# Optimization experiments

Hardware: AMD Instinct MI355X
Metric: run time of the kernel (lower is better)

The kernel has to match this reference:

```python
import jax, jax.numpy as jnp
import numpy as np

LAM = 1.0
N_ITERS = 20
TOL = 1e-6


def setup_inputs() -> dict:
    key = jax.random.key(0)
    k0, k1, k2, k3, k4 = jax.random.split(key, 5)
    B, M, d, E, a = 8, 50000, 8, 800000, 8
    c0 = jax.random.normal(k0, (B, M, d), dtype=jnp.float32)
    src = jax.random.randint(k1, (E,), 0, M, dtype=jnp.int32)
    dst = jax.random.randint(k2, (E,), 0, M, dtype=jnp.int32)
    R_src = jax.random.normal(k3, (E, a, d), dtype=jnp.float32)
    R_dst = jax.random.normal(k4, (E, a, d), dtype=jnp.float32)
    return {"c0": c0, "src": src, "dst": dst, "R_src": R_src, "R_dst": R_dst}


def _batch_dot(x, y):
    # [B,M,d] x [B,M,d] -> [B,1,1]
    return jnp.sum(x * y, axis=(1, 2), keepdims=True)


def _matvec(p, src, dst, R_src, R_dst):
    # p: [B,M,d] -> p + lam * L p via per-edge gather-einsum-scatter
    r = (jnp.einsum('ead,bed->bea', R_src, p[:, src, :])
         - jnp.einsum('ead,bed->bea', R_dst, p[:, dst, :]))  # [B,E,a]
    c_src = jnp.einsum('ead,bea->bed', R_src, r)   # [B,E,d]
    c_dst = -jnp.einsum('ead,bea->bed', R_dst, r)  # [B,E,d]
    acc = jnp.zeros_like(p).at[:, src, :].add(c_src).at[:, dst, :].add(c_dst)
    return p + LAM * acc


def _cg_solve(b, x0, src, dst, R_src, R_dst):
    mv = lambda q: _matvec(q, src, dst, R_src, R_dst)
    x = x0
    r = b - mv(x)
    p = r
    rsold = _batch_dot(r, r)
    done = jnp.array(False)

    def body(i, state):
        x, r, p, rsold, done = state
        Ap = mv(p)
        alpha = rsold / (_batch_dot(p, Ap) + 1e-12)
        x_new = x + alpha * p
        r_new = r - alpha * Ap
        rsnew = _batch_dot(r_new, r_new)
        conv = jnp.sqrt(jnp.mean(rsnew)) < TOL  # torch breaks AFTER updating x,r
        p_new = r_new + rsnew / (rsold + 1e-12) * p
        x = jnp.where(done, x, x_new)
        r = jnp.where(done, r, r_new)
        frozen = done | conv
        p = jnp.where(frozen, p, p_new)
        rsold = jnp.where(frozen, rsold, rsnew)
        return (x, r, p, rsold, frozen)

    x, _, _, _, _ = jax.lax.fori_loop(0, N_ITERS, body, (x, r, p, rsold, done))
    return x


def reference(c0, src, dst, R_src, R_dst):
    c0_f = c0.astype(jnp.float32)
    c = _cg_solve(c0_f, c0_f, src, dst, R_src, R_dst)
    return c.astype(c0.dtype)
```

## Files before the change

### kernel.cpp

```cpp
#include <hip/hip_runtime.h>
#include <math.h>

constexpr float LAM = 1.0f;
constexpr int   NIT = 20;
constexpr float TOL = 1e-6f;

typedef float f4 __attribute__((ext_vector_type(4)));

#define S_RSOLD 0
#define S_ALPHA 8
#define S_BETA  16
#define S_FLAG  24
#define S_PAP   32
#define S_RS    (32+2048)
#define SCAL_F  (32+4096)

__device__ __forceinline__ float dot8v(f4 a0, f4 a1, f4 b0, f4 b1){
  return a0[0]*b0[0] + a0[1]*b0[1] + a0[2]*b0[2] + a0[3]*b0[3]
       + a1[0]*b1[0] + a1[1]*b1[1] + a1[2]*b1[2] + a1[3]*b1[3];
}

__global__ void k_setup_nm(float* __restrict__ scal, int* __restrict__ cursor, int Mn){
  int i = blockIdx.x * blockDim.x + threadIdx.x;
  int stride = gridDim.x * blockDim.x;
  for (int j = i; j < SCAL_F; j += stride) scal[j] = 0.f;
  for (int j = i; j < Mn; j += stride) cursor[j] = 0;
}

__global__ void k_deg(const int* __restrict__ src, const int* __restrict__ dst,
                      int* __restrict__ cnt, int E){
  int i = blockIdx.x * blockDim.x + threadIdx.x;
  int stride = gridDim.x * blockDim.x;
  for (int e = i; e < E; e += stride){
    atomicAdd(&cnt[src[e]], 1);
    atomicAdd(&cnt[dst[e]], 1);
  }
}

__global__ void k_scan(int* __restrict__ cnt, int* __restrict__ rowptr,
                       int* __restrict__ cursor, int Mn, int tot){
  __shared__ int sm[1024];
  const int T = 1024;
  int t = threadIdx.x;
  int chunk = (Mn + T - 1) / T;
  int lo = t * chunk, hi = lo + chunk; if (hi > Mn) hi = Mn;
  int s = 0;
  for (int i = lo; i < hi; ++i) s += cnt[i];
  sm[t] = s;
  __syncthreads();
  for (int o = 1; o < T; o <<= 1){
    int v = (t >= o) ? sm[t - o] : 0;
    __syncthreads();
    sm[t] += v;
    __syncthreads();
  }
  int base = (t == 0) ? 0 : sm[t - 1];
  for (int i = lo; i < hi; ++i){
    int c = cnt[i];
    rowptr[i] = base;
    cursor[i] = base;
    base += c;
  }
  if (t == T - 1) rowptr[Mn] = tot;
}

__global__ void k_fill(const int* __restrict__ src, const int* __restrict__ dst,
                       int* __restrict__ cursor, int* __restrict__ col,
                       int* __restrict__ es, int E){
  int i = blockIdx.x * blockDim.x + threadIdx.x;
  int stride = gridDim.x * blockDim.x;
  for (int e = i; e < E; e += stride){
    int s = src[e], t = dst[e];
    int ps = atomicAdd(&cursor[s], 1);
    col[ps] = t; es[ps] = (e << 1);
    int pt = atomicAdd(&cursor[t], 1);
    col[pt] = s; es[pt] = (e << 1) | 1;
  }
}

__global__ void k_medge(const float* __restrict__ Rs, const float* __restrict__ Rd,
                        float* __restrict__ Mb, int E){
  int g  = blockIdx.x * blockDim.x + threadIdx.x;
  int wv = g >> 6, l = g & 63;
  int nw = (gridDim.x * blockDim.x) >> 6;
  int d1 = l >> 3, d2 = l & 7;
  for (int e = wv; e < E; e += nw){
    float rs = Rs[(size_t)e * 64 + l];
    float rd = Rd[(size_t)e * 64 + l];
    float Mm = 0.f;
    #pragma unroll
    for (int a = 0; a < 8; ++a)
      Mm += __shfl(rs, a * 8 + d1, 64) * __shfl(rd, a * 8 + d2, 64);
    Mb[(size_t)e * 64 + l] = Mm;
  }
}

__global__ void k_buildd(const float* __restrict__ Rs, const float* __restrict__ Rd,
                         const int* __restrict__ rowptr, const int* __restrict__ es,
                         float* __restrict__ Dd, int v0, int v1){
  int g = blockIdx.x * blockDim.x + threadIdx.x;
  int v = v0 + (g >> 6);
  if (v >= v1) return;
  int l = g & 63, d1 = l >> 3, d2 = l & 7;
  float Dacc = 0.f;
  int j0 = rowptr[v], j1 = rowptr[v + 1];
  int j = j0;
  for (; j + 2 <= j1; j += 2){
    int e0 = es[j], e1 = es[j + 1];
    const float* R0 = (e0 & 1) ? Rd : Rs;
    const float* R1 = (e1 & 1) ? Rd : Rs;
    float x0 = R0[(size_t)(e0 >> 1) * 64 + l];
    float x1 = R1[(size_t)(e1 >> 1) * 64 + l];
    #pragma unroll
    for (int a = 0; a < 8; ++a){
      float p0 = __shfl(x0, a * 8 + d1, 64);
      float s0 = __shfl(x0, a * 8 + d2, 64);
      float p1 = __shfl(x1, a * 8 + d1, 64);
      float s1 = __shfl(x1, a * 8 + d2, 64);
      Dacc += p0 * s0 + p1 * s1;
    }
  }
  for (; j < j1; ++j){
    int e0 = es[j];
    const float* R0 = (e0 & 1) ? Rd : Rs;
    float x0 = R0[(size_t)(e0 >> 1) * 64 + l];
    #pragma unroll
    for (int a = 0; a < 8; ++a)
      Dacc += __shfl(x0, a * 8 + d1, 64) * __shfl(x0, a * 8 + d2, 64);
  }
  Dd[(size_t)v * 64 + l] = ((d1 == d2) ? 1.f : 0.f) + LAM * Dacc;
}

__global__ void k_mv(const float* __restrict__ Mb, const float* __restrict__ Dd,
                     const int* __restrict__ rowptr, const int* __restrict__ col,
                     const int* __restrict__ es, const float* __restrict__ p,
                     float* __restrict__ out, float* __restrict__ scal, int Mn){
  if (*(const int*)(scal + S_FLAG)) return;
  __shared__ float pbuf[4][8][68];
  __shared__ float mbuf[4][8][68];
  __shared__ int   cbuf[4][128];
  __shared__ int   ebuf[4][128];
  int g = blockIdx.x * blockDim.x + threadIdx.x;
  int v = g >> 6;
  if (v >= Mn) return;
  int w  = threadIdx.x >> 6;
  int l  = g & 63;
  int hi = l >> 3, lo = l & 7;
  int k8 = lo * 8;
  int b8 = hi * 8;
  int j0 = rowptr[v];
  int rowlen = rowptr[v + 1] - j0;

  for (int jj = l; jj < rowlen && jj < 128; jj += 64){
    cbuf[w][jj] = col[j0 + jj];
    ebuf[w][jj] = es[j0 + jj];
  }

  int nch = (rowlen + 7) >> 3;

  auto gaddr = [&](int n, int& c, int& e){
    int jj = n * 8 + hi;
    c = v; e = 0;
    if (jj < rowlen){
      if (jj < 128){ c = cbuf[w][jj]; e = ebuf[w][jj] >> 1; }
      else         { c = col[j0 + jj]; e = es[j0 + jj] >> 1; }
    }
  };

  const f4* pv4 = (const f4*)(p + (size_t)v * 64 + b8);
  f4 pv0 = pv4[0], pv1 = pv4[1];
  const f4* dr4 = (const f4*)(Dd + (size_t)v * 64 + k8);
  float acc = dot8v(dr4[0], dr4[1], pv0, pv1);

  f4 gp0, gp1, gm0, gm1;
  if (nch > 0){
    int c, e; gaddr(0, c, e);
    const float* pc = p + (size_t)c * 64 + k8;
    gp0 = *(const f4*)pc; gp1 = *(const f4*)(pc + 4);
    const float* mc = Mb + (size_t)e * 64 + k8;
    gm0 = *(const f4*)mc; gm1 = *(const f4*)(mc + 4);
  }

  for (int n = 0; n < nch; ++n){
    float* dp = &pbuf[w][hi][k8];
    *(f4*)dp = gp0; *(f4*)(dp + 4) = gp1;
    float* dm = &mbuf[w][hi][k8];
    *(f4*)dm = gm0; *(f4*)(dm + 4) = gm1;
    bool more = (n + 1 < nch);
    if (more){
      int c, e; gaddr(n + 1, c, e);
      const float* pc = p + (size_t)c * 64 + k8;
      gp0 = *(const f4*)pc; gp1 = *(const f4*)(pc + 4);
      const float* mc = Mb + (size_t)e * 64 + k8;
      gm0 = *(const f4*)mc; gm1 = *(const f4*)(mc + 4);
    }
    int jb = n * 8;
    int lim = rowlen - jb;
    if (lim >= 8){
      #pragma unroll
      for (int q = 0; q < 8; ++q){
        int jj = jb + q;
        int sd = ((jj < 128) ? ebuf[w][jj] : es[j0 + jj]) & 1;
        const float* pr = &pbuf[w][q][b8];
        f4 q0 = *(const f4*)pr, q1 = *(const f4*)(pr + 4);
        const float* mc = &mbuf[w][q][0];
        if (!sd){
          f4 m0 = *(const f4*)(mc + k8);
          f4 m1 = *(const f4*)(mc + k8 + 4);
          acc -= LAM * dot8v(m0, m1, q0, q1);
        } else {
          acc -= LAM * ( mc[lo]      * q0[0] + mc[lo +  8] * q0[1]
                       + mc[lo + 16] * q0[2] + mc[lo + 24] * q0[3]
                       + mc[lo + 32] * q1[0] + mc[lo + 40] * q1[1]
                       + mc[lo + 48] * q1[2] + mc[lo + 56] * q1[3]);
        }
      }
    } else {
      #pragma unroll
      for (int q = 0; q < 8; ++q){
        if (q < lim){
          int jj = jb + q;
          int sd = ((jj < 128) ? ebuf[w][jj] : es[j0 + jj]) & 1;
          const float* pr = &pbuf[w][q][b8];
          f4 q0 = *(const f4*)pr, q1 = *(const f4*)(pr + 4);
          const float* mc = &mbuf[w][q][0];
          if (!sd){
            f4 m0 = *(const f4*)(mc + k8);
            f4 m1 = *(const f4*)(mc + k8 + 4);
            acc -= LAM * dot8v(m0, m1, q0, q1);
          } else {
            acc -= LAM * ( mc[lo]      * q0[0] + mc[lo +  8] * q0[1]
                         + mc[lo + 16] * q0[2] + mc[lo + 24] * q0[3]
                         + mc[lo + 32] * q1[0] + mc[lo + 40] * q1[1]
                         + mc[lo + 48] * q1[2] + mc[lo + 56] * q1[3]);
          }
        }
      }
    }
  }
  out[(size_t)v * 64 + l] = acc;
  float pself = (lo & 4) ? ((lo & 2) ? ((lo & 1) ? pv1[3] : pv1[2])
                                     : ((lo & 1) ? pv1[1] : pv1[0]))
                         : ((lo & 2) ? ((lo & 1) ? pv0[3] : pv0[2])
                                     : ((lo & 1) ? pv0[1] : pv0[0]));
  float part = pself * acc;
  part += __shfl_xor(part, 1, 64);
  part += __shfl_xor(part, 2, 64);
  part += __shfl_xor(part, 4, 64);
  if (lo == 0)
    atomicAdd(&scal[S_PAP + hi * 256 + (blockIdx.x & 255)], part);
}

__global__ void k_perm(const float* __restrict__ c0, float* __restrict__ xp, int Mn){
  int i = blockIdx.x * blockDim.x + threadIdx.x;
  int n4 = Mn * 16;
  if (i >= n4) return;
  int v = i >> 4, rem = i & 15, b = rem >> 1, half = rem & 1;
  f4 cv = *(const f4*)(c0 + ((size_t)b * Mn + v) * 8 + half * 4);
  ((f4*)xp)[i] = cv;
}

__global__ void k_init_nm(float* __restrict__ p, const float* __restrict__ Ap,
                          float* __restrict__ r, float* __restrict__ x_bm,
                          float* __restrict__ scal, int n4tot, int Mn){
  int i = blockIdx.x * blockDim.x + threadIdx.x;
  int l = threadIdx.x & 63;
  float part = 0.f;
  if (i < n4tot){
    f4 cv = ((const f4*)p)[i];
    f4 av = ((const f4*)Ap)[i];
    f4 rv = cv - av;
    ((f4*)r)[i] = rv;
    ((f4*)p)[i] = rv;
    int v = i >> 4, rem = i & 15, b = rem >> 1, half = rem & 1;
    ((f4*)x_bm)[((size_t)b * Mn + v) * 2 + half] = cv;
    part = rv[0]*rv[0] + rv[1]*rv[1] + rv[2]*rv[2] + rv[3]*rv[3];
  }
  part += __shfl_xor(part, 1, 64);
  part += __shfl_xor(part, 16, 64);
  part += __shfl_xor(part, 32, 64);
  if ((l & 49) == 0)
    atomicAdd(&scal[S_RS + ((l >> 1) & 7) * 256 + (blockIdx.x & 255)], part);
}

__global__ void k_s0(float* __restrict__ scal){
  __shared__ float sm[256];
  int t = threadIdx.x;
  int b = t >> 5, k0 = t & 31;
  float s = 0.f;
  #pragma unroll
  for (int i = 0; i < 8; ++i) s += scal[S_RS + b * 256 + k0 + i * 32];
  sm[t] = s;
  __syncthreads();
  if (t < 8){
    float tot = 0.f;
    #pragma unroll
    for (int i = 0; i < 32; ++i) tot += sm[t * 32 + i];
    scal[S_RSOLD + t] = tot;
  }
  __syncthreads();
  for (int i = t; i < 4096; i += 256) scal[S_PAP + i] = 0.f;
}

__global__ void k_upd_nm(float* __restrict__ x_bm, float* __restrict__ r,
                         const float* __restrict__ p, const float* __restrict__ Ap,
                         float* __restrict__ scal, int n4tot, int Mn){
  if (*(const int*)(scal + S_FLAG)) return;
  __shared__ float sal[8];
  int t = threadIdx.x;
  if (t < 8){
    float s = 0.f;
    const float* pp = scal + S_PAP + t * 256;
    #pragma unroll 4
    for (int k = 0; k < 256; ++k) s += pp[k];
    sal[t] = scal[S_RSOLD + t] / (s + 1e-12f);
  }
  __syncthreads();
  int i = blockIdx.x * blockDim.x + t;
  int l = t & 63;
  float part = 0.f;
  if (i < n4tot){
    int v = i >> 4, rem = i & 15, b = rem >> 1, half = rem & 1;
    float al = sal[b];
    size_t xi = ((size_t)b * Mn + v) * 2 + half;
    f4 pv = ((const f4*)p)[i];
    f4 av = ((const f4*)Ap)[i];
    f4 xv = ((f4*)x_bm)[xi];
    f4 rv = ((f4*)r)[i];
    xv += al * pv;
    rv -= al * av;
    ((f4*)x_bm)[xi] = xv;
    ((f4*)r)[i] = rv;
    part = rv[0]*rv[0] + rv[1]*rv[1] + rv[2]*rv[2] + rv[3]*rv[3];
  }
  part += __shfl_xor(part, 1, 64);
  part += __shfl_xor(part, 16, 64);
  part += __shfl_xor(part, 32, 64);
  if ((l & 49) == 0)
    atomicAdd(&scal[S_RS + ((l >> 1) & 7) * 256 + (blockIdx.x & 255)], part);
}

__global__ void k_s2(float* __restrict__ scal){
  if (*(const int*)(scal + S_FLAG)) return;
  __shared__ float sm[256];
  __shared__ float rsn[8];
  int t = threadIdx.x;
  int b = t >> 5, k0 = t & 31;
  float s = 0.f;
  #pragma unroll
  for (int i = 0; i < 8; ++i) s += scal[S_RS + b * 256 + k0 + i * 32];
  sm[t] = s;
  __syncthreads();
  if (t < 8){
    float tot = 0.f;
    #pragma unroll
    for (int i = 0; i < 32; ++i) tot += sm[t * 32 + i];
    rsn[t] = tot;
  }
  __syncthreads();
  if (t == 0){
    float ssum = 0.f;
    for (int bb = 0; bb < 8; ++bb) ssum += rsn[bb];
    if (sqrtf(ssum / 8.0f) < TOL){
      *(int*)(scal + S_FLAG) = 1;
    } else {
      for (int bb = 0; bb < 8; ++bb){
        scal[S_BETA + bb]  = rsn[bb] / (scal[S_RSOLD + bb] + 1e-12f);
        scal[S_RSOLD + bb] = rsn[bb];
      }
    }
  }
  __syncthreads();
  for (int i = t; i < 4096; i += 256) scal[S_PAP + i] = 0.f;
}

__global__ void k_pupd_nm(const float* __restrict__ r, float* __restrict__ p,
                          const float* __restrict__ scal, int n4tot){
  if (*(const int*)(scal + S_FLAG)) return;
  int i = blockIdx.x * blockDim.x + threadIdx.x;
  if (i >= n4tot) return;
  int b = (i >> 1) & 7;
  float be = scal[S_BETA + b];
  f4 rv = ((const f4*)r)[i];
  f4 pv = ((f4*)p)[i];
  pv = rv + be * pv;
  ((f4*)p)[i] = pv;
}

#define OS_RSOLD 0
#define OS_PAP   8
#define OS_RSNEW 16
#define OS_ALPHA 24
#define OS_BETA  32
#define OS_FLAG  40

__device__ __forceinline__ float blk_reduce_256(float v){
  __shared__ float sm[4];
  #pragma unroll
  for (int o = 32; o > 0; o >>= 1) v += __shfl_down(v, o, 64);
  int lane = threadIdx.x & 63, w = threadIdx.x >> 6;
  if (lane == 0) sm[w] = v;
  __syncthreads();
  return (threadIdx.x == 0) ? (sm[0] + sm[1] + sm[2] + sm[3]) : 0.f;
}

__global__ void k_setup_fb(float* scal){
  int i = blockIdx.x * blockDim.x + threadIdx.x;
  if (i < 64) scal[i] = 0.f;
}

__global__ void k_apinit(const float* __restrict__ in, float* __restrict__ out,
                         int n4tot, const int* __restrict__ flag){
  if (*flag) return;
  int j = blockIdx.x * blockDim.x + threadIdx.x;
  if (j < n4tot) ((f4*)out)[j] = ((const f4*)in)[j];
}

__global__ void k_mv_edge_fb(const float* __restrict__ Rs, const float* __restrict__ Rd,
                             const int* __restrict__ src, const int* __restrict__ dst,
                             const float* __restrict__ in, float* __restrict__ out,
                             int Mn, int E, const int* __restrict__ flag){
  if (*flag) return;
  int g  = blockIdx.x * blockDim.x + threadIdx.x;
  int wv = g >> 6, l = g & 63;
  int nw = (gridDim.x * blockDim.x) >> 6;
  int b = l >> 3, q = l & 7;
  for (int e = wv; e < E; e += nw){
    int s = src[e], t = dst[e];
    const f4* rs4 = (const f4*)(Rs + (size_t)e * 64 + q * 8);
    const f4* rd4 = (const f4*)(Rd + (size_t)e * 64 + q * 8);
    const f4* ps4 = (const f4*)(in + ((size_t)b * Mn + s) * 8);
    const f4* pd4 = (const f4*)(in + ((size_t)b * Mn + t) * 8);
    f4 ra0 = rs4[0], ra1 = rs4[1], pa0 = ps4[0], pa1 = ps4[1];
    f4 rb0 = rd4[0], rb1 = rd4[1], pb0 = pd4[0], pb1 = pd4[1];
    float re = dot8v(ra0, ra1, pa0, pa1) - dot8v(rb0, rb1, pb0, pb1);
    float cs = 0.f, cd = 0.f;
    #pragma unroll
    for (int a = 0; a < 8; ++a){
      float rea = __shfl(re, b * 8 + a, 64);
      cs += Rs[(size_t)e * 64 + a * 8 + q] * rea;
      cd += Rd[(size_t)e * 64 + a * 8 + q] * rea;
    }
    atomicAdd(&out[((size_t)b * Mn + s) * 8 + q],  LAM * cs);
    atomicAdd(&out[((size_t)b * Mn + t) * 8 + q], -LAM * cd);
  }
}

__global__ void k_init_o(const float* __restrict__ c0, const float* __restrict__ Ap,
                         float* __restrict__ x, float* __restrict__ r, float* __restrict__ p,
                         float* scal, int n4){
  int b = blockIdx.y;
  size_t base = (size_t)b * n4;
  int j = blockIdx.x * blockDim.x + threadIdx.x;
  float part = 0.f;
  if (j < n4){
    f4 cv = ((const f4*)c0)[base + j];
    f4 av = ((const f4*)Ap)[base + j];
    f4 rv = cv - av;
    ((f4*)x)[base + j] = cv;
    ((f4*)r)[base + j] = rv;
    ((f4*)p)[base + j] = rv;
    part = rv[0]*rv[0] + rv[1]*rv[1] + rv[2]*rv[2] + rv[3]*rv[3];
  }
  float tot = blk_reduce_256(part);
  if (threadIdx.x == 0) atomicAdd(&scal[OS_RSOLD + b], tot);
}

__global__ void k_dot_o(const float* __restrict__ p, const float* __restrict__ Ap,
                        float* scal, int n4){
  const int* flag = (const int*)(scal + OS_FLAG);
  if (*flag) return;
  int b = blockIdx.y;
  size_t base = (size_t)b * n4;
  int j = blockIdx.x * blockDim.x + threadIdx.x;
  float part = 0.f;
  if (j < n4){
    f4 pv = ((const f4*)p)[base + j];
    f4 av = ((const f4*)Ap)[base + j];
    part = pv[0]*av[0] + pv[1]*av[1] + pv[2]*av[2] + pv[3]*av[3];
  }
  float tot = blk_reduce_256(part);
  if (threadIdx.x == 0) atomicAdd(&scal[OS_PAP + b], tot);
}

__global__ void k_s1_o(float* scal){
  const int* flag = (const int*)(scal + OS_FLAG);
  if (*flag) return;
  int t = threadIdx.x;
  if (t < 8){
    scal[OS_ALPHA + t] = scal[OS_RSOLD + t] / (scal[OS_PAP + t] + 1e-12f);
    scal[OS_RSNEW + t] = 0.f;
  }
}

__global__ void k_upd_o(float* __restrict__ x, float* __restrict__ r,
                        const float* __restrict__ p, const float* __restrict__ Ap,
                        float* scal, int n4){
  const int* flag = (const int*)(scal + OS_FLAG);
  if (*flag) return;
  int b = blockIdx.y;
  size_t base = (size_t)b * n4;
  float al = scal[OS_ALPHA + b];
  int j = blockIdx.x * blockDim.x + threadIdx.x;
  float part = 0.f;
  if (j < n4){
    f4 pv = ((const f4*)p)[base + j];
    f4 av = ((const f4*)Ap)[base + j];
    f4 xv = ((f4*)x)[base + j];
    f4 rv = ((f4*)r)[base + j];
    xv += al * pv;
    rv -= al * av;
    ((f4*)x)[base + j] = xv;
    ((f4*)r)[base + j] = rv;
    part = rv[0]*rv[0] + rv[1]*rv[1] + rv[2]*rv[2] + rv[3]*rv[3];
  }
  float tot = blk_reduce_256(part);
  if (threadIdx.x == 0) atomicAdd(&scal[OS_RSNEW + b], tot);
}

__global__ void k_s2_o(float* scal){
  int* flag = (int*)(scal + OS_FLAG);
  if (*flag) return;
  if (threadIdx.x == 0){
    float ssum = 0.f;
    for (int bb = 0; bb < 8; ++bb) ssum += scal[OS_RSNEW + bb];
    if (sqrtf(ssum / 8.0f) < TOL){
      *flag = 1;
    } else {
      for (int bb = 0; bb < 8; ++bb){
        scal[OS_BETA + bb]  = scal[OS_RSNEW + bb] / (scal[OS_RSOLD + bb] + 1e-12f);
        scal[OS_RSOLD + bb] = scal[OS_RSNEW + bb];
        scal[OS_PAP + bb]   = 0.f;
      }
    }
  }
}

__global__ void k_pupd_o(const float* __restrict__ r, float* __restrict__ p,
                         float* scal, int n4){
  const int* flag = (const int*)(scal + OS_FLAG);
  if (*flag) return;
  int b = blockIdx.y;
  size_t base = (size_t)b * n4;
  float be = scal[OS_BETA + b];
  int j = blockIdx.x * blockDim.x + threadIdx.x;
  if (j < n4){
    f4 rv = ((const f4*)r)[base + j];
    f4 pv = ((f4*)p)[base + j];
    pv = rv + be * pv;
    ((f4*)p)[base + j] = pv;
  }
}

extern "C" void kernel_launch(void* const* d_in, const int* in_sizes, int n_in,
                              void* d_out, int out_size, void* d_ws, size_t ws_size,
                              hipStream_t stream){
  const float* c0  = (const float*)d_in[0];
  const int*   src = (const int*)d_in[1];
  const int*   dst = (const int*)d_in[2];
  const float* Rs  = (const float*)d_in[3];
  const float* Rd  = (const float*)d_in[4];

  int N  = in_sizes[0];
  int Mn = N / 64;
  int E  = in_sizes[1];
  int n4tot = N / 4;
  int twoE = 2 * E;

  float* ws = (float*)d_ws;
  size_t off = 0;
  float* r    = ws + off;  off += N;
  float* p    = ws + off;  off += N;
  float* Ap   = ws + off;  off += N;
  float* scal = ws + off;  off += SCAL_F;
  float* Dd   = ws + off;  off += (size_t)Mn * 64;
  int* rowptr = (int*)(ws + off);  off += (size_t)((Mn + 1 + 3) & ~3);
  int* cursor = (int*)(ws + off);  off += (size_t)((Mn + 3) & ~3);
  int* colA   = (int*)(ws + off);  off += (size_t)twoE;
  int* esA    = (int*)(ws + off);  off += (size_t)twoE;
  float* Mb   = ws + off;  off += (size_t)E * 64;
  size_t need_main = off * 4;

  int nb_vec  = (n4tot + 255) / 256;
  int nb_node = (Mn * 64 + 255) / 256;

  if (ws_size >= need_main){
    k_setup_nm<<<512, 256, 0, stream>>>(scal, cursor, Mn);
    k_deg  <<<1024, 256, 0, stream>>>(src, dst, cursor, E);
    k_scan <<<1, 1024, 0, stream>>>(cursor, rowptr, cursor, Mn, twoE);
    k_fill <<<1024, 256, 0, stream>>>(src, dst, cursor, colA, esA, E);
    k_medge<<<4096, 256, 0, stream>>>(Rs, Rd, Mb, E);
    int Mh = (Mn + 1) / 2;
    int nb_h1 = (Mh * 64 + 255) / 256;
    int nb_h2 = ((Mn - Mh) * 64 + 255) / 256;
    k_buildd<<<nb_h1, 256, 0, stream>>>(Rs, Rd, rowptr, esA, Dd, 0, Mh);
    k_buildd<<<nb_h2, 256, 0, stream>>>(Rs, Rd, rowptr, esA, Dd, Mh, Mn);

    float* x_bm = (float*)d_out;
    k_perm<<<nb_vec, 256, 0, stream>>>(c0, p, Mn);
    k_mv<<<nb_node, 256, 0, stream>>>(Mb, Dd, rowptr, colA, esA, p, Ap, scal, Mn);
    k_init_nm<<<nb_vec, 256, 0, stream>>>(p, Ap, r, x_bm, scal, n4tot, Mn);
    k_s0<<<1, 256, 0, stream>>>(scal);

    for (int it = 0; it < NIT; ++it){
      k_mv<<<nb_node, 256, 0, stream>>>(Mb, Dd, rowptr, colA, esA, p, Ap, scal, Mn);
      k_upd_nm<<<nb_vec, 256, 0, stream>>>(x_bm, r, p, Ap, scal, n4tot, Mn);
      k_s2<<<1, 256, 0, stream>>>(scal);
      k_pupd_nm<<<nb_vec, 256, 0, stream>>>(r, p, scal, n4tot);
    }
  } else {
    float* fr    = ws;
    float* fp    = fr + N;
    float* fAp   = fp + N;
    float* fscal = fAp + N;
    const int* flagp = (const int*)(fscal + OS_FLAG);
    int n4 = Mn * 2;
    dim3 vgrid((n4 + 255) / 256, 8);
    int cb = (n4tot + 255) / 256;
    float* x = (float*)d_out;

    k_setup_fb<<<1, 64, 0, stream>>>(fscal);
    k_apinit<<<cb, 256, 0, stream>>>(c0, fAp, n4tot, flagp);
    k_mv_edge_fb<<<2048, 256, 0, stream>>>(Rs, Rd, src, dst, c0, fAp, Mn, E, flagp);
    k_init_o<<<vgrid, 256, 0, stream>>>(c0, fAp, x, fr, fp, fscal, n4);
    for (int it = 0; it < NIT; ++it){
      k_apinit<<<cb, 256, 0, stream>>>(fp, fAp, n4tot, flagp);
      k_mv_edge_fb<<<2048, 256, 0, stream>>>(Rs, Rd, src, dst, fp, fAp, Mn, E, flagp);
      k_dot_o<<<vgrid, 256, 0, stream>>>(fp, fAp, fscal, n4);
      k_s1_o<<<1, 64, 0, stream>>>(fscal);
      k_upd_o<<<vgrid, 256, 0, stream>>>(x, fr, fp, fAp, fscal, n4);
      k_s2_o<<<1, 64, 0, stream>>>(fscal);
      k_pupd_o<<<vgrid, 256, 0, stream>>>(fr, fp, fscal, n4);
    }
  }
}
```

Before: 5.086 ms.

## Fuse per-edge M and diagonal block construction with atomic scatter

Replaces the separate edge-coupling kernel and the two per-node CSR diagonal-build kernels with one per-edge kernel. It reads R_src/R_dst once, computes the coupling block plus both self-blocks, and atomically adds the self-blocks into the node diagonal. The diagonal is initialised to identity in the setup kernel. Mb is also written and read with nontemporal hints to reduce cache pollution in the matvec. This trades a second gather pass over R for float atomics, which adds contention and makes the summation order nondeterministic.

```diff
diff --git a/kernel.cpp b/kernel.cpp
--- a/kernel.cpp
+++ b/kernel.cpp
@@ -20,11 +20,15 @@
        + a1[0]*b1[0] + a1[1]*b1[1] + a1[2]*b1[2] + a1[3]*b1[3];
 }
 
-__global__ void k_setup_nm(float* __restrict__ scal, int* __restrict__ cursor, int Mn){
+__global__ void k_setup_nm(float* __restrict__ D, float* __restrict__ scal,
+                           int* __restrict__ cursor, int Mn){
   int i = blockIdx.x * blockDim.x + threadIdx.x;
   int stride = gridDim.x * blockDim.x;
   for (int j = i; j < SCAL_F; j += stride) scal[j] = 0.f;
   for (int j = i; j < Mn; j += stride) cursor[j] = 0;
+  int tot = Mn * 64;
+  for (int j = i; j < tot; j += stride)
+    D[j] = (((j >> 3) & 7) == (j & 7)) ? 1.f : 0.f;
 }
 
 __global__ void k_deg(const int* __restrict__ src, const int* __restrict__ dst,
@@ -78,8 +82,9 @@
   }
 }
 
-__global__ void k_medge(const float* __restrict__ Rs, const float* __restrict__ Rd,
-                        float* __restrict__ Mb, int E){
+__global__ void k_edgeM(const float* __restrict__ Rs, const float* __restrict__ Rd,
+                        const int* __restrict__ src, const int* __restrict__ dst,
+                        float* __restrict__ Mb, float* __restrict__ D, int E){
   int g  = blockIdx.x * blockDim.x + threadIdx.x;
   int wv = g >> 6, l = g & 63;
   int nw = (gridDim.x * blockDim.x) >> 6;
@@ -87,48 +92,22 @@
   for (int e = wv; e < E; e += nw){
     float rs = Rs[(size_t)e * 64 + l];
     float rd = Rd[(size_t)e * 64 + l];
-    float Mm = 0.f;
-    #pragma unroll
-    for (int a = 0; a < 8; ++a)
-      Mm += __shfl(rs, a * 8 + d1, 64) * __shfl(rd, a * 8 + d2, 64);
-    Mb[(size_t)e * 64 + l] = Mm;
-  }
-}
-
-__global__ void k_buildd(const float* __restrict__ Rs, const float* __restrict__ Rd,
-                         const int* __restrict__ rowptr, const int* __restrict__ es,
-                         float* __restrict__ Dd, int v0, int v1){
-  int g = blockIdx.x * blockDim.x + threadIdx.x;
-  int v = v0 + (g >> 6);
-  if (v >= v1) return;
-  int l = g & 63, d1 = l >> 3, d2 = l & 7;
-  float Dacc = 0.f;
-  int j0 = rowptr[v], j1 = rowptr[v + 1];
-  int j = j0;
-  for (; j + 2 <= j1; j += 2){
-    int e0 = es[j], e1 = es[j + 1];
-    const float* R0 = (e0 & 1) ? Rd : Rs;
-    const float* R1 = (e1 & 1) ? Rd : Rs;
-    float x0 = R0[(size_t)(e0 >> 1) * 64 + l];
-    float x1 = R1[(size_t)(e1 >> 1) * 64 + l];
+    float As = 0.f, Ad = 0.f, Mm = 0.f;
     #pragma unroll
     for (int a = 0; a < 8; ++a){
-      float p0 = __shfl(x0, a * 8 + d1, 64);
-      float s0 = __shfl(x0, a * 8 + d2, 64);
-      float p1 = __shfl(x1, a * 8 + d1, 64);
-      float s1 = __shfl(x1, a * 8 + d2, 64);
-      Dacc += p0 * s0 + p1 * s1;
-    }
-  }
-  for (; j < j1; ++j){
-    int e0 = es[j];
-    const float* R0 = (e0 & 1) ? Rd : Rs;
-    float x0 = R0[(size_t)(e0 >> 1) * 64 + l];
-    #pragma unroll
-    for (int a = 0; a < 8; ++a)
-      Dacc += __shfl(x0, a * 8 + d1, 64) * __shfl(x0, a * 8 + d2, 64);
-  }
-  Dd[(size_t)v * 64 + l] = ((d1 == d2) ? 1.f : 0.f) + LAM * Dacc;
+      float s1 = __shfl(rs, a * 8 + d1, 64);
+      float s2 = __shfl(rs, a * 8 + d2, 64);
+      float t1 = __shfl(rd, a * 8 + d1, 64);
+      float t2 = __shfl(rd, a * 8 + d2, 64);
+      As += s1 * s2;
+      Ad += t1 * t2;
+      Mm += s1 * t2;
+    }
+    __builtin_nontemporal_store(Mm, &Mb[(size_t)e * 64 + l]);
+    int s = src[e], t = dst[e];
+    atomicAdd(&D[(size_t)s * 64 + l], LAM * As);
+    atomicAdd(&D[(size_t)t * 64 + l], LAM * Ad);
+  }
 }
 
 __global__ void k_mv(const float* __restrict__ Mb, const float* __restrict__ Dd,
@@ -177,8 +156,9 @@
     int c, e; gaddr(0, c, e);
     const float* pc = p + (size_t)c * 64 + k8;
     gp0 = *(const f4*)pc; gp1 = *(const f4*)(pc + 4);
-    const float* mc = Mb + (size_t)e * 64 + k8;
-    gm0 = *(const f4*)mc; gm1 = *(const f4*)(mc + 4);
+    const f4* mc = (const f4*)(Mb + (size_t)e * 64 + k8);
+    gm0 = __builtin_nontemporal_load(mc);
+    gm1 = __builtin_nontemporal_load(mc + 1);
   }
 
   for (int n = 0; n < nch; ++n){
@@ -191,8 +171,9 @@
       int c, e; gaddr(n + 1, c, e);
       const float* pc = p + (size_t)c * 64 + k8;
       gp0 = *(const f4*)pc; gp1 = *(const f4*)(pc + 4);
-      const float* mc = Mb + (size_t)e * 64 + k8;
-      gm0 = *(const f4*)mc; gm1 = *(const f4*)(mc + 4);
+      const f4* mc = (const f4*)(Mb + (size_t)e * 64 + k8);
+      gm0 = __builtin_nontemporal_load(mc);
+      gm1 = __builtin_nontemporal_load(mc + 1);
     }
     int jb = n * 8;
     int lim = rowlen - jb;
@@ -585,16 +566,11 @@
   int nb_node = (Mn * 64 + 255) / 256;
 
   if (ws_size >= need_main){
-    k_setup_nm<<<512, 256, 0, stream>>>(scal, cursor, Mn);
+    k_setup_nm<<<2048, 256, 0, stream>>>(Dd, scal, cursor, Mn);
     k_deg  <<<1024, 256, 0, stream>>>(src, dst, cursor, E);
     k_scan <<<1, 1024, 0, stream>>>(cursor, rowptr, cursor, Mn, twoE);
     k_fill <<<1024, 256, 0, stream>>>(src, dst, cursor, colA, esA, E);
-    k_medge<<<4096, 256, 0, stream>>>(Rs, Rd, Mb, E);
-    int Mh = (Mn + 1) / 2;
-    int nb_h1 = (Mh * 64 + 255) / 256;
-    int nb_h2 = ((Mn - Mh) * 64 + 255) / 256;
-    k_buildd<<<nb_h1, 256, 0, stream>>>(Rs, Rd, rowptr, esA, Dd, 0, Mh);
-    k_buildd<<<nb_h2, 256, 0, stream>>>(Rs, Rd, rowptr, esA, Dd, Mh, Mn);
+    k_edgeM<<<4096, 256, 0, stream>>>(Rs, Rd, src, dst, Mb, Dd, E);
 
     float* x_bm = (float*)d_out;
     k_perm<<<nb_vec, 256, 0, stream>>>(c0, p, Mn);
```

New measurement: 5.448 ms. +7.1%, slower.
